# Kernel optimization log

Measured on AMD Instinct MI355X. Metric: run time of the kernel, lower is better.

## Reference

```python
import jax, jax.numpy as jnp
import numpy as np

B, IN, HID, OUT, E, K = 16384, 512, 1024, 512, 16, 4


def setup_inputs() -> dict:
    key = jax.random.key(0)
    k0, k1, k2, k3 = jax.random.split(key, 4)
    return {
        "x": jax.random.normal(k0, (B, IN), jnp.float32),
        "w_gate": jax.random.normal(k1, (IN, E), jnp.float32) * 0.02,
        "w1": jax.random.normal(k2, (E, IN, HID), jnp.float32) * (1.0 / np.sqrt(IN)),
        "b1": jnp.zeros((E, HID), jnp.float32),
        "w2": jax.random.normal(k3, (E, HID, OUT), jnp.float32) * (1.0 / np.sqrt(HID)),
        "b2": jnp.zeros((E, OUT), jnp.float32),
    }


def _top_k_gating(x, w_gate):
    # Eval-mode (no noise) noisy_top_k_gating: logits -> top-(k+1) -> softmax over top-k
    logits = x @ w_gate  # [B, E]
    m = min(K + 1, E)
    top_logits, top_idx = jax.lax.top_k(logits, m)  # [B, m]
    tk_logits = top_logits[:, :K]                    # [B, K]
    tk_idx = top_idx[:, :K]                          # [B, K] int32
    tk_gates = jax.nn.softmax(tk_logits, axis=1)     # softmax over the k selected
    rows = jnp.arange(logits.shape[0])[:, None]
    gates = jnp.zeros_like(logits).at[rows, tk_idx].set(tk_gates)  # sparse [B, E]
    return gates


def reference(x, w_gate, w1, b1, w2, b2):
    # Gating
    gates = _top_k_gating(x, w_gate)  # [B, E], zero for non-selected experts
    # Dispatch/combine: output[b] = sum_e gates[b,e] * MLP_e(x[b]).
    # Torch code only evaluates experts on selected rows; since gates are exactly
    # zero elsewhere, the dense weighted sum below computes identical math.
    y = jnp.zeros((x.shape[0], w2.shape[2]), x.dtype)
    for e in range(E):  # fixed small expert count; each iter is one grouped GEMM pair
        h = jax.nn.relu(x @ w1[e] + b1[e])                 # [B, HID]
        o = jax.nn.softmax(h @ w2[e] + b2[e], axis=1)      # expert MLP ends in Softmax(dim=1)
        y = y + gates[:, e:e + 1] * o
    return y
```

## Files before the change

### kernel.cpp

```cpp
#include <hip/hip_runtime.h>
#include <hip/hip_fp16.h>

typedef _Float16 f16;
typedef _Float16 f16x8 __attribute__((ext_vector_type(8)));
typedef float f32x4 __attribute__((ext_vector_type(4)));

#define MFMA(a,b,c) __builtin_amdgcn_mfma_f32_16x16x32_f16((a),(b),(c),0,0,0)

#define BAR() do { \
  asm volatile("s_waitcnt lgkmcnt(0)" ::: "memory"); \
  __builtin_amdgcn_sched_barrier(0); \
  __builtin_amdgcn_s_barrier(); \
  __builtin_amdgcn_sched_barrier(0); \
} while (0)


__global__ void k_cvt_w1(const float* __restrict__ w1, f16* __restrict__ w1fr) {
  int fid = blockIdx.x * 4 + (threadIdx.x >> 6);
  int l = threadIdx.x & 63;
  int e = fid >> 10, n0 = (fid >> 4) & 63, kc = fid & 15;
  int kbase = kc * 32 + (l >> 4) * 8;
  int col = n0 * 16 + (l & 15);
  const float* src = w1 + ((size_t)e * 512 + kbase) * 1024 + col;
  f16x8 o;
  #pragma unroll
  for (int i = 0; i < 8; i++) o[i] = (f16)src[(size_t)i * 1024];
  *(f16x8*)(w1fr + (size_t)fid * 512 + l * 8) = o;
}

__global__ void k_cvt_w2(const float* __restrict__ w2, f16* __restrict__ w2fr) {
  int fid = blockIdx.x * 4 + (threadIdx.x >> 6);
  int l = threadIdx.x & 63;
  int e = fid >> 10, n0 = (fid >> 5) & 31, kc = fid & 31;
  int kbase = kc * 32 + (l >> 4) * 8;
  int col = n0 * 16 + (l & 15);
  const float* src = w2 + ((size_t)e * 1024 + kbase) * 512 + col;
  f16x8 o;
  #pragma unroll
  for (int i = 0; i < 8; i++) o[i] = (f16)src[(size_t)i * 512];
  *(f16x8*)(w2fr + (size_t)fid * 512 + l * 8) = o;
}

__global__ void k_gate(const float* __restrict__ x, const float* __restrict__ wg,
                       int* __restrict__ tk_idx, float* __restrict__ tk_gate) {
  int w = threadIdx.x >> 6, l = threadIdx.x & 63;
  int r = blockIdx.x * 4 + w;
  float p[16];
  #pragma unroll
  for (int e = 0; e < 16; e++) p[e] = 0.f;
  const float* xr = x + (size_t)r * 512;
  #pragma unroll
  for (int t = 0; t < 8; t++) {
    float xv = xr[t * 64 + l];
    const float* wrow = wg + (t * 64 + l) * 16;
    #pragma unroll
    for (int e = 0; e < 16; e++) p[e] += xv * wrow[e];
  }
  #pragma unroll
  for (int e = 0; e < 16; e++) {
    float v = p[e];
    #pragma unroll
    for (int m = 32; m >= 1; m >>= 1) v += __shfl_xor(v, m);
    p[e] = v;
  }
  unsigned chosen = 0;
  float bv[4]; int bi[4];
  #pragma unroll
  for (int j = 0; j < 4; j++) {
    float best = -3.4e38f; int be = 0;
    #pragma unroll
    for (int e = 0; e < 16; e++) {
      bool ok = !((chosen >> e) & 1u) && (p[e] > best);
      if (ok) { best = p[e]; be = e; }
    }
    chosen |= 1u << be; bv[j] = best; bi[j] = be;
  }
  float m0 = bv[0];
  float e0 = __expf(bv[0] - m0), e1 = __expf(bv[1] - m0),
        e2 = __expf(bv[2] - m0), e3 = __expf(bv[3] - m0);
  float s = e0 + e1 + e2 + e3;
  if (l == 0) {
    *(int4*)(tk_idx + (size_t)r * 4) = make_int4(bi[0], bi[1], bi[2], bi[3]);
    *(float4*)(tk_gate + (size_t)r * 4) = make_float4(e0 / s, e1 / s, e2 / s, e3 / s);
  }
}

__global__ void k_route_count(const int* __restrict__ tk_idx, int* __restrict__ partial) {
  int e = blockIdx.x >> 6, chunk = blockIdx.x & 63;
  int t = threadIdx.x;
  int row = chunk * 256 + t;
  int4 tk = ((const int4*)tk_idx)[row];
  bool match = (tk.x == e) || (tk.y == e) || (tk.z == e) || (tk.w == e);
  unsigned long long m = __ballot(match);
  __shared__ int wc[4];
  if ((t & 63) == 0) wc[t >> 6] = (int)__popcll(m);
  __syncthreads();
  if (t == 0) partial[e * 64 + chunk] = wc[0] + wc[1] + wc[2] + wc[3];
}

__global__ void k_route_scan(const int* __restrict__ partial, int* __restrict__ chunk_base,
                             int* __restrict__ count) {
  int l = threadIdx.x;
  for (int e = 0; e < 16; e++) {
    int v = partial[e * 64 + l];
    int orig = v;
    #pragma unroll
    for (int off = 1; off < 64; off <<= 1) {
      int u = __shfl_up(v, off);
      if (l >= off) v += u;
    }
    chunk_base[e * 64 + l] = v - orig;
    if (l == 63) count[e] = v;
  }
}

__global__ void k_route_scatter(const int* __restrict__ tk_idx, const float* __restrict__ tk_gate,
                                const int* __restrict__ chunk_base, int* __restrict__ rows_pk,
                                float* __restrict__ gates_l) {
  int e = blockIdx.x >> 6, chunk = blockIdx.x & 63;
  int t = threadIdx.x, w = t >> 6, l = t & 63;
  int row = chunk * 256 + t;
  int4 tk = ((const int4*)tk_idx)[row];
  int j = (tk.x == e) ? 0 : (tk.y == e) ? 1 : (tk.z == e) ? 2 : (tk.w == e) ? 3 : -1;
  bool match = (j >= 0);
  unsigned long long m = __ballot(match);
  __shared__ int wc[4];
  if (l == 0) wc[w] = (int)__popcll(m);
  __syncthreads();
  int wbase = 0;
  #pragma unroll
  for (int i = 0; i < 4; i++) if (i < w) wbase += wc[i];
  if (match) {
    int pos = (int)__popcll(m & ((1ULL << l) - 1ULL));
    int idx = e * 16384 + chunk_base[e * 64 + chunk] + wbase + pos;
    rows_pk[idx] = row | (j << 16);
    gates_l[idx] = tk_gate[(size_t)row * 4 + j];
  }
}

__global__ void k_zero(float4* __restrict__ y4) {
  y4[blockIdx.x * 256 + threadIdx.x] = make_float4(0.f, 0.f, 0.f, 0.f);
}

__global__ __launch_bounds__(512, 2) void k_expert(
    const float* __restrict__ x, const f16* __restrict__ w1fr, const f16* __restrict__ w2fr,
    const float* __restrict__ b1, const float* __restrict__ b2,
    const int* __restrict__ count, const int* __restrict__ rows_pk,
    const float* __restrict__ gates_l, float* __restrict__ y)
{
  int p = blockIdx.x;
  int xcd = p & 7, s = p >> 3;
  int e = (xcd << 1) | (s >> 8);
  int rb = s & 255;
  int cnt = count[e];
  int mstart = rb * 64;
  if (mstart >= cnt) return;
  int nvalid = cnt - mstart; if (nvalid > 64) nvalid = 64;

  __shared__ f16 x_lds[64 * 512];
  __shared__ f16 h_lds[64 * 512];
  __shared__ int rowarr[64];
  __shared__ float gatearr[64];
  __shared__ float red[2][8][64];

  int t = threadIdx.x, w = t >> 6, l = t & 63;
  int lq = l >> 4, lr = l & 15;

  if (t < 64) {
    int idx = (t < nvalid) ? t : (nvalid - 1);
    int src = e * 16384 + mstart + idx;
    rowarr[t] = rows_pk[src];
    gatearr[t] = gates_l[src];
  }
  BAR();

  char* xb = (char*)x_lds;
  char* hb = (char*)h_lds;

  {
    int srow = t >> 3, sj = t & 7;
    const float* sp = x + (size_t)(rowarr[srow] & 0xFFFF) * 512;
    #pragma unroll
    for (int j = 0; j < 8; j++) {
      int seg = sj + j * 8;
      const float* qp = sp + seg * 8;
      float4 u0 = ((const float4*)qp)[0], u1 = ((const float4*)qp)[1];
      f16x8 v;
      v[0]=(f16)u0.x; v[1]=(f16)u0.y; v[2]=(f16)u0.z; v[3]=(f16)u0.w;
      v[4]=(f16)u1.x; v[5]=(f16)u1.y; v[6]=(f16)u1.z; v[7]=(f16)u1.w;
      int byte = srow * 1024 + ((seg ^ srow) & 63) * 16;
      *(f16x8*)(xb + byte) = v;
    }
  }
  BAR();

  const f16x8* w1f8 = (const f16x8*)w1fr;
  const f16x8* w2f8 = (const f16x8*)w2fr;

  f32x4 acc2[4][4];
  #pragma unroll
  for (int a = 0; a < 4; a++)
    #pragma unroll
    for (int b = 0; b < 4; b++)
      #pragma unroll
      for (int q = 0; q < 4; q++) acc2[a][b][q] = 0.f;

  #pragma unroll 1
  for (int hc = 0; hc < 2; hc++) {
    f32x4 acc1[4][4];
    #pragma unroll
    for (int a = 0; a < 4; a++)
      #pragma unroll
      for (int b = 0; b < 4; b++)
        #pragma unroll
        for (int q = 0; q < 4; q++) acc1[a][b][q] = 0.f;

    const f16x8* bp1 = w1f8 + ((size_t)((e * 64 + hc * 32 + w * 4) * 16)) * 64 + l;
    #pragma unroll 4
    for (int kcg = 0; kcg < 16; kcg++) {
      f16x8 bf0 = bp1[kcg * 64];
      f16x8 bf1 = bp1[16 * 64 + kcg * 64];
      f16x8 bf2 = bp1[32 * 64 + kcg * 64];
      f16x8 bf3 = bp1[48 * 64 + kcg * 64];
      int seg = kcg * 4 + lq;
      f16x8 av[4];
      #pragma unroll
      for (int mf = 0; mf < 4; mf++) {
        int row = mf * 16 + lr;
        av[mf] = *(const f16x8*)(xb + row * 1024 + ((seg ^ row) & 63) * 16);
      }
      #pragma unroll
      for (int mf = 0; mf < 4; mf++) {
        acc1[mf][0] = MFMA(av[mf], bf0, acc1[mf][0]);
        acc1[mf][1] = MFMA(av[mf], bf1, acc1[mf][1]);
        acc1[mf][2] = MFMA(av[mf], bf2, acc1[mf][2]);
        acc1[mf][3] = MFMA(av[mf], bf3, acc1[mf][3]);
      }
    }

    BAR();
    #pragma unroll
    for (int nf = 0; nf < 4; nf++) {
      int cc = w * 64 + nf * 16 + lr;
      float bv = b1[e * 1024 + hc * 512 + cc];
      int segw = cc >> 3;
      int inb = (cc & 7) * 2;
      #pragma unroll
      for (int mf = 0; mf < 4; mf++)
        #pragma unroll
        for (int q = 0; q < 4; q++) {
          int row = mf * 16 + lq * 4 + q;
          float hv = fmaxf(acc1[mf][nf][q] + bv, 0.f);
          int byte = row * 1024 + ((segw ^ row) & 63) * 16 + inb;
          *(f16*)(hb + byte) = (f16)hv;
        }
    }
    BAR();

    const f16x8* bp2 = w2f8 + ((size_t)((e * 32 + w * 4) * 32 + hc * 16)) * 64 + l;
    #pragma unroll 4
    for (int kc2 = 0; kc2 < 16; kc2++) {
      f16x8 wf0 = bp2[kc2 * 64];
      f16x8 wf1 = bp2[32 * 64 + kc2 * 64];
      f16x8 wf2 = bp2[64 * 64 + kc2 * 64];
      f16x8 wf3 = bp2[96 * 64 + kc2 * 64];
      int seg = kc2 * 4 + lq;
      f16x8 av[4];
      #pragma unroll
      for (int mf = 0; mf < 4; mf++) {
        int row = mf * 16 + lr;
        av[mf] = *(const f16x8*)(hb + row * 1024 + ((seg ^ row) & 63) * 16);
      }
      #pragma unroll
      for (int mf = 0; mf < 4; mf++) {
        acc2[mf][0] = MFMA(av[mf], wf0, acc2[mf][0]);
        acc2[mf][1] = MFMA(av[mf], wf1, acc2[mf][1]);
        acc2[mf][2] = MFMA(av[mf], wf2, acc2[mf][2]);
        acc2[mf][3] = MFMA(av[mf], wf3, acc2[mf][3]);
      }
    }
  }

  #pragma unroll
  for (int nf = 0; nf < 4; nf++) {
    float bv = b2[e * 512 + w * 64 + nf * 16 + lr];
    #pragma unroll
    for (int mf = 0; mf < 4; mf++)
      #pragma unroll
      for (int q = 0; q < 4; q++) acc2[mf][nf][q] += bv;
  }

  float rmax[4][4];
  #pragma unroll
  for (int mf = 0; mf < 4; mf++)
    #pragma unroll
    for (int q = 0; q < 4; q++) {
      float v = acc2[mf][0][q];
      #pragma unroll
      for (int nf = 1; nf < 4; nf++) v = fmaxf(v, acc2[mf][nf][q]);
      #pragma unroll
      for (int m = 1; m < 16; m <<= 1) v = fmaxf(v, __shfl_xor(v, m));
      rmax[mf][q] = v;
    }
  if (lr == 0) {
    #pragma unroll
    for (int mf = 0; mf < 4; mf++)
      #pragma unroll
      for (int q = 0; q < 4; q++) red[0][w][mf * 16 + lq * 4 + q] = rmax[mf][q];
  }
  BAR();
  float gmax[4][4];
  #pragma unroll
  for (int mf = 0; mf < 4; mf++)
    #pragma unroll
    for (int q = 0; q < 4; q++) {
      int row = mf * 16 + lq * 4 + q;
      float v = red[0][0][row];
      #pragma unroll
      for (int ww = 1; ww < 8; ww++) v = fmaxf(v, red[0][ww][row]);
      gmax[mf][q] = v;
    }
  float psum[4][4];
  #pragma unroll
  for (int mf = 0; mf < 4; mf++)
    #pragma unroll
    for (int q = 0; q < 4; q++) psum[mf][q] = 0.f;
  #pragma unroll
  for (int mf = 0; mf < 4; mf++)
    #pragma unroll
    for (int nf = 0; nf < 4; nf++)
      #pragma unroll
      for (int q = 0; q < 4; q++) {
        float pp = __expf(acc2[mf][nf][q] - gmax[mf][q]);
        acc2[mf][nf][q] = pp;
        psum[mf][q] += pp;
      }
  #pragma unroll
  for (int mf = 0; mf < 4; mf++)
    #pragma unroll
    for (int q = 0; q < 4; q++) {
      float v = psum[mf][q];
      #pragma unroll
      for (int m = 1; m < 16; m <<= 1) v += __shfl_xor(v, m);
      psum[mf][q] = v;
    }
  if (lr == 0) {
    #pragma unroll
    for (int mf = 0; mf < 4; mf++)
      #pragma unroll
      for (int q = 0; q < 4; q++) red[1][w][mf * 16 + lq * 4 + q] = psum[mf][q];
  }
  BAR();

  #pragma unroll
  for (int mf = 0; mf < 4; mf++) {
    #pragma unroll
    for (int q = 0; q < 4; q++) {
      int row = mf * 16 + lq * 4 + q;
      if (row < nvalid) {
        float ssum = 0.f;
        #pragma unroll
        for (int ww = 0; ww < 8; ww++) ssum += red[1][ww][row];
        float sc = gatearr[row] / ssum;
        int orow = rowarr[row] & 0xFFFF;
        float* yr = y + (size_t)orow * 512 + w * 64 + lr;
        #pragma unroll
        for (int nf = 0; nf < 4; nf++) {
          atomicAdd(yr + nf * 16, acc2[mf][nf][q] * sc);
        }
      }
    }
  }
}

extern "C" void kernel_launch(void* const* d_in, const int* in_sizes, int n_in,
                              void* d_out, int out_size, void* d_ws, size_t ws_size,
                              hipStream_t stream) {
  (void)in_sizes; (void)n_in; (void)out_size; (void)ws_size;
  const float* x  = (const float*)d_in[0];
  const float* wg = (const float*)d_in[1];
  const float* w1 = (const float*)d_in[2];
  const float* b1 = (const float*)d_in[3];
  const float* w2 = (const float*)d_in[4];
  const float* b2 = (const float*)d_in[5];
  float* y = (float*)d_out;

  char* ws = (char*)d_ws;
  size_t off = 0;
  auto alloc = [&](size_t bytes) -> char* {
    char* p = ws + off;
    off += (bytes + 255) & ~(size_t)255;
    return p;
  };
  f16*   w1fr       = (f16*)  alloc((size_t)16 * 512 * 1024 * 2);
  f16*   w2fr       = (f16*)  alloc((size_t)16 * 1024 * 512 * 2);
  int*   tk_idx     = (int*)  alloc((size_t)16384 * 4 * 4);
  float* tk_gate    = (float*)alloc((size_t)16384 * 4 * 4);
  int*   rows_pk    = (int*)  alloc((size_t)16 * 16384 * 4);
  float* gates_l    = (float*)alloc((size_t)16 * 16384 * 4);
  int*   partial    = (int*)  alloc(16 * 64 * 4);
  int*   chunk_base = (int*)  alloc(16 * 64 * 4);
  int*   count      = (int*)  alloc(256);

  k_cvt_w1<<<dim3(4096), dim3(256), 0, stream>>>(w1, w1fr);
  k_cvt_w2<<<dim3(4096), dim3(256), 0, stream>>>(w2, w2fr);
  k_gate<<<dim3(4096), dim3(256), 0, stream>>>(x, wg, tk_idx, tk_gate);
  k_route_count<<<dim3(1024), dim3(256), 0, stream>>>(tk_idx, partial);
  k_route_scan<<<dim3(1), dim3(64), 0, stream>>>(partial, chunk_base, count);
  k_route_scatter<<<dim3(1024), dim3(256), 0, stream>>>(tk_idx, tk_gate, chunk_base,
                                                        rows_pk, gates_l);
  k_zero<<<dim3(8192), dim3(256), 0, stream>>>((float4*)y);
  k_expert<<<dim3(4096), dim3(512), 0, stream>>>(x, w1fr, w2fr, b1, b2,
                                                 count, rows_pk, gates_l, y);
}
```

Baseline: 387.0 us.

## Split hidden dim into four chunks and software-pipeline weight loads in expert GEMMs

The expert kernel now processes the hidden dimension in four 256-wide chunks instead of two 512-wide ones. This halves the h LDS buffer and the acc1 register tile, with a new XOR swizzle for the smaller row stride. Both GEMM loops now prefetch weight fragments into rotating register slots (4 slots for GEMM1, 2 for GEMM2) so global loads for later k-steps are issued while MFMAs consume earlier ones. The aim is lower LDS and register use, which may raise occupancy, plus hidden global-load latency. The cost is twice as many barrier-separated phases per block.

```diff
diff --git a/kernel.cpp b/kernel.cpp
--- a/kernel.cpp
+++ b/kernel.cpp
@@ -158,7 +158,7 @@
   int nvalid = cnt - mstart; if (nvalid > 64) nvalid = 64;
 
   __shared__ f16 x_lds[64 * 512];
-  __shared__ f16 h_lds[64 * 512];
+  __shared__ f16 h_lds[64 * 256];
   __shared__ int rowarr[64];
   __shared__ float gatearr[64];
   __shared__ float red[2][8][64];
@@ -206,43 +206,50 @@
       for (int q = 0; q < 4; q++) acc2[a][b][q] = 0.f;
 
   #pragma unroll 1
-  for (int hc = 0; hc < 2; hc++) {
-    f32x4 acc1[4][4];
+  for (int hc = 0; hc < 4; hc++) {
+    f32x4 acc1[4][2];
     #pragma unroll
     for (int a = 0; a < 4; a++)
       #pragma unroll
-      for (int b = 0; b < 4; b++)
+      for (int b = 0; b < 2; b++)
         #pragma unroll
         for (int q = 0; q < 4; q++) acc1[a][b][q] = 0.f;
 
-    const f16x8* bp1 = w1f8 + ((size_t)((e * 64 + hc * 32 + w * 4) * 16)) * 64 + l;
-    #pragma unroll 4
-    for (int kcg = 0; kcg < 16; kcg++) {
-      f16x8 bf0 = bp1[kcg * 64];
-      f16x8 bf1 = bp1[16 * 64 + kcg * 64];
-      f16x8 bf2 = bp1[32 * 64 + kcg * 64];
-      f16x8 bf3 = bp1[48 * 64 + kcg * 64];
-      int seg = kcg * 4 + lq;
-      f16x8 av[4];
-      #pragma unroll
-      for (int mf = 0; mf < 4; mf++) {
-        int row = mf * 16 + lr;
-        av[mf] = *(const f16x8*)(xb + row * 1024 + ((seg ^ row) & 63) * 16);
-      }
-      #pragma unroll
-      for (int mf = 0; mf < 4; mf++) {
-        acc1[mf][0] = MFMA(av[mf], bf0, acc1[mf][0]);
-        acc1[mf][1] = MFMA(av[mf], bf1, acc1[mf][1]);
-        acc1[mf][2] = MFMA(av[mf], bf2, acc1[mf][2]);
-        acc1[mf][3] = MFMA(av[mf], bf3, acc1[mf][3]);
-      }
-    }
+    const f16x8* bp1 = w1f8 + ((size_t)((e * 64 + hc * 16 + w * 2) * 16)) * 64 + l;
+    #define LD1(dst, k) { dst[0] = bp1[(k) * 64]; dst[1] = bp1[16 * 64 + (k) * 64]; }
+    #define ST1(slot, kk) { \
+      int seg = (kk) * 4 + lq; \
+      f16x8 av0 = *(const f16x8*)(xb + (lr) * 1024 + ((seg ^ lr) & 63) * 16); \
+      f16x8 av1 = *(const f16x8*)(xb + (16 + lr) * 1024 + ((seg ^ (16 + lr)) & 63) * 16); \
+      f16x8 av2 = *(const f16x8*)(xb + (32 + lr) * 1024 + ((seg ^ (32 + lr)) & 63) * 16); \
+      f16x8 av3 = *(const f16x8*)(xb + (48 + lr) * 1024 + ((seg ^ (48 + lr)) & 63) * 16); \
+      acc1[0][0] = MFMA(av0, slot[0], acc1[0][0]); \
+      acc1[0][1] = MFMA(av0, slot[1], acc1[0][1]); \
+      acc1[1][0] = MFMA(av1, slot[0], acc1[1][0]); \
+      acc1[1][1] = MFMA(av1, slot[1], acc1[1][1]); \
+      acc1[2][0] = MFMA(av2, slot[0], acc1[2][0]); \
+      acc1[2][1] = MFMA(av2, slot[1], acc1[2][1]); \
+      acc1[3][0] = MFMA(av3, slot[0], acc1[3][0]); \
+      acc1[3][1] = MFMA(av3, slot[1], acc1[3][1]); \
+    }
+    f16x8 wA[2], wB[2], wC[2], wD[2];
+    LD1(wA, 0) LD1(wB, 1) LD1(wC, 2) LD1(wD, 3)
+    #pragma unroll 1
+    for (int j = 0; j < 4; j++) {
+      int kb = j * 4;
+      ST1(wA, kb + 0); if (j < 3) LD1(wA, kb + 4);
+      ST1(wB, kb + 1); if (j < 3) LD1(wB, kb + 5);
+      ST1(wC, kb + 2); if (j < 3) LD1(wC, kb + 6);
+      ST1(wD, kb + 3); if (j < 3) LD1(wD, kb + 7);
+    }
+    #undef LD1
+    #undef ST1
 
     BAR();
     #pragma unroll
-    for (int nf = 0; nf < 4; nf++) {
-      int cc = w * 64 + nf * 16 + lr;
-      float bv = b1[e * 1024 + hc * 512 + cc];
+    for (int nf = 0; nf < 2; nf++) {
+      int cc = w * 32 + nf * 16 + lr;
+      float bv = b1[e * 1024 + hc * 256 + cc];
       int segw = cc >> 3;
       int inb = (cc & 7) * 2;
       #pragma unroll
@@ -251,34 +258,52 @@
         for (int q = 0; q < 4; q++) {
           int row = mf * 16 + lq * 4 + q;
           float hv = fmaxf(acc1[mf][nf][q] + bv, 0.f);
-          int byte = row * 1024 + ((segw ^ row) & 63) * 16 + inb;
+          int byte = row * 512 + ((segw ^ (row & 31)) & 31) * 16 + inb;
           *(f16*)(hb + byte) = (f16)hv;
         }
     }
     BAR();
 
-    const f16x8* bp2 = w2f8 + ((size_t)((e * 32 + w * 4) * 32 + hc * 16)) * 64 + l;
-    #pragma unroll 4
-    for (int kc2 = 0; kc2 < 16; kc2++) {
-      f16x8 wf0 = bp2[kc2 * 64];
-      f16x8 wf1 = bp2[32 * 64 + kc2 * 64];
-      f16x8 wf2 = bp2[64 * 64 + kc2 * 64];
-      f16x8 wf3 = bp2[96 * 64 + kc2 * 64];
-      int seg = kc2 * 4 + lq;
-      f16x8 av[4];
-      #pragma unroll
-      for (int mf = 0; mf < 4; mf++) {
-        int row = mf * 16 + lr;
-        av[mf] = *(const f16x8*)(hb + row * 1024 + ((seg ^ row) & 63) * 16);
-      }
-      #pragma unroll
-      for (int mf = 0; mf < 4; mf++) {
-        acc2[mf][0] = MFMA(av[mf], wf0, acc2[mf][0]);
-        acc2[mf][1] = MFMA(av[mf], wf1, acc2[mf][1]);
-        acc2[mf][2] = MFMA(av[mf], wf2, acc2[mf][2]);
-        acc2[mf][3] = MFMA(av[mf], wf3, acc2[mf][3]);
-      }
-    }
+    const f16x8* bp2 = w2f8 + ((size_t)((e * 32 + w * 4) * 32 + hc * 8)) * 64 + l;
+    #define LD2(dst, k) { \
+      dst[0] = bp2[(k) * 64]; \
+      dst[1] = bp2[32 * 64 + (k) * 64]; \
+      dst[2] = bp2[64 * 64 + (k) * 64]; \
+      dst[3] = bp2[96 * 64 + (k) * 64]; \
+    }
+    #define ST2(slot, kk) { \
+      int seg = (kk) * 4 + lq; \
+      f16x8 av0 = *(const f16x8*)(hb + (lr) * 512 + (((seg) ^ (lr & 31)) & 31) * 16); \
+      f16x8 av1 = *(const f16x8*)(hb + (16 + lr) * 512 + (((seg) ^ ((16 + lr) & 31)) & 31) * 16); \
+      f16x8 av2 = *(const f16x8*)(hb + (32 + lr) * 512 + (((seg) ^ ((32 + lr) & 31)) & 31) * 16); \
+      f16x8 av3 = *(const f16x8*)(hb + (48 + lr) * 512 + (((seg) ^ ((48 + lr) & 31)) & 31) * 16); \
+      acc2[0][0] = MFMA(av0, slot[0], acc2[0][0]); \
+      acc2[0][1] = MFMA(av0, slot[1], acc2[0][1]); \
+      acc2[0][2] = MFMA(av0, slot[2], acc2[0][2]); \
+      acc2[0][3] = MFMA(av0, slot[3], acc2[0][3]); \
+      acc2[1][0] = MFMA(av1, slot[0], acc2[1][0]); \
+      acc2[1][1] = MFMA(av1, slot[1], acc2[1][1]); \
+      acc2[1][2] = MFMA(av1, slot[2], acc2[1][2]); \
+      acc2[1][3] = MFMA(av1, slot[3], acc2[1][3]); \
+      acc2[2][0] = MFMA(av2, slot[0], acc2[2][0]); \
+      acc2[2][1] = MFMA(av2, slot[1], acc2[2][1]); \
+      acc2[2][2] = MFMA(av2, slot[2], acc2[2][2]); \
+      acc2[2][3] = MFMA(av2, slot[3], acc2[2][3]); \
+      acc2[3][0] = MFMA(av3, slot[0], acc2[3][0]); \
+      acc2[3][1] = MFMA(av3, slot[1], acc2[3][1]); \
+      acc2[3][2] = MFMA(av3, slot[2], acc2[3][2]); \
+      acc2[3][3] = MFMA(av3, slot[3], acc2[3][3]); \
+    }
+    f16x8 uA[4], uB[4];
+    LD2(uA, 0) LD2(uB, 1)
+    #pragma unroll 1
+    for (int j = 0; j < 4; j++) {
+      int kb = j * 2;
+      ST2(uA, kb + 0); if (j < 3) LD2(uA, kb + 2);
+      ST2(uB, kb + 1); if (j < 3) LD2(uB, kb + 3);
+    }
+    #undef LD2
+    #undef ST2
   }
 
   #pragma unroll
```

Result: faster. 372.2 us (-3.8%).
